# Optimization experiments

Hardware: AMD Instinct MI355X
Metric: run time of the kernel (lower is better)

The kernel has to match this reference:

```python
import jax, jax.numpy as jnp
import numpy as np

HEADS = 16  # init kwarg 'heads'

def setup_inputs() -> dict:
    key = jax.random.key(0)
    k1, k2, k3 = jax.random.split(key, 3)
    B, S, D = 2, 2048, 1024
    x = jax.random.normal(k1, (B, S, D), dtype=jnp.float32)
    # nn.Linear(dim, 3*dim, bias=False): y = x @ W^T; store as [D, 3D] already transposed.
    w_qkv = jax.random.normal(k2, (D, 3 * D), dtype=jnp.float32) * 0.02
    w_out = jax.random.normal(k3, (D, D), dtype=jnp.float32) * 0.02
    return {"x": x, "w_qkv": w_qkv, "w_out": w_out}

def reference(x, w_qkv, w_out):
    B, S, D = x.shape
    H = HEADS
    hd = D // H
    scale = 1.0 / jnp.sqrt(jnp.asarray(hd, dtype=x.dtype))
    qkv = x @ w_qkv                      # [B, S, 3D]
    q, k, v = jnp.split(qkv, 3, axis=-1)
    def to_heads(t):
        return t.reshape(B, S, H, hd).transpose(0, 2, 1, 3)  # [B, H, S, hd]
    q, k, v = to_heads(q), to_heads(k), to_heads(v)
    scores = jnp.einsum('bhqd,bhkd->bhqk', q, k) * scale      # [B, H, S, S]
    # causal mask: query i attends to keys j <= i
    causal = jnp.tril(jnp.ones((S, S), dtype=bool))
    scores = jnp.where(causal, scores, -jnp.inf)
    p = jax.nn.softmax(scores, axis=-1)  # online-softmax in the original == exact softmax
    o = jnp.einsum('bhqk,bhkd->bhqd', p, v)                   # [B, H, S, hd]
    out = o.transpose(0, 2, 1, 3).reshape(B, S, D)
    return out @ w_out
```

## Files before the change

### kernel.cpp

```cpp
#include <hip/hip_runtime.h>


typedef unsigned short u16;
typedef unsigned int   u32;
typedef __attribute__((ext_vector_type(4))) u16    u16x4;
typedef __attribute__((ext_vector_type(8))) u16    u16x8;
typedef __attribute__((ext_vector_type(4))) short  s16x4;
typedef __attribute__((ext_vector_type(8))) __bf16 bf16x8;
typedef __attribute__((ext_vector_type(4))) float  f32x4;
typedef __attribute__((ext_vector_type(16))) float f32x16;

#define DEV static __device__ __forceinline__

DEV u16 f2b(float f) {
  unsigned u = __float_as_uint(f);
  u += 0x7fffu + ((u >> 16) & 1u);
  return (u16)(u >> 16);
}

DEV void gload_lds16(const void* g, void* l) {
  __builtin_amdgcn_global_load_lds((const __attribute__((address_space(1))) void*)g,
                                   (__attribute__((address_space(3))) void*)l, 16, 0, 0);
}

DEV unsigned lds_off(const void* p) {
  return (unsigned)(unsigned long long)(const __attribute__((address_space(3))) void*)p;
}

DEV s16x4 tr_read(unsigned off) {
  s16x4 d;
  asm volatile("ds_read_b64_tr_b16 %0, %1" : "=v"(d) : "v"(off));
  return d;
}

DEV u32 cvt_pk(float lo, float hi) {
  u32 r;
  asm("v_cvt_pk_bf16_f32 %0, %1, %2" : "=v"(r) : "v"(lo), "v"(hi));
  return r;
}

DEV void pswap(u32& x, u32& y) {
  asm volatile("v_permlane32_swap_b32 %0, %1" : "+v"(x), "+v"(y));
}

DEV f32x4 mfma32(bf16x8 a, bf16x8 b, f32x4 c) {
  return __builtin_amdgcn_mfma_f32_16x16x32_bf16(a, b, c, 0, 0, 0);
}
DEV f32x16 mfma3232(bf16x8 a, bf16x8 b, f32x16 c) {
  return __builtin_amdgcn_mfma_f32_32x32x16_bf16(a, b, c, 0, 0, 0);
}

__global__ __launch_bounds__(256) void cvt_kernel(const float* __restrict__ in,
                                                  u16* __restrict__ out, int n4) {
  int i = blockIdx.x * 256 + threadIdx.x;
  if (i >= n4) return;
  const float4 v = ((const float4*)in)[i];
  u16x4 o = { f2b(v.x), f2b(v.y), f2b(v.z), f2b(v.w) };
  ((u16x4*)out)[i] = o;
}

__global__ __launch_bounds__(256) void transpose_cvt(const float* __restrict__ w,
                                                     u16* __restrict__ wt,
                                                     const int Kdim, const int Ndim,
                                                     const int scaleN) {
  __shared__ u16 ls[32][33];
  const int tn = blockIdx.x * 32, tk = blockIdx.y * 32;
  const int t = threadIdx.x;
  const int r = t >> 3, c4 = (t & 7) * 4;
  const float s = (tn < scaleN) ? 0.18033688011112042f : 1.0f;
  float4 v = *(const float4*)(w + (size_t)(tk + r) * Ndim + tn + c4);
  ls[r][c4 + 0] = f2b(v.x * s); ls[r][c4 + 1] = f2b(v.y * s);
  ls[r][c4 + 2] = f2b(v.z * s); ls[r][c4 + 3] = f2b(v.w * s);
  __syncthreads();
  u16x4 ov = { ls[c4 + 0][r], ls[c4 + 1][r], ls[c4 + 2][r], ls[c4 + 3][r] };
  *(u16x4*)(wt + (size_t)(tn + r) * Kdim + tk + c4) = ov;
}

template<bool OUT_BF16>
__global__ __launch_bounds__(256) void gemm_bt(const u16* __restrict__ A,
                                               const u16* __restrict__ Bt,
                                               void* __restrict__ C, const int ldc) {
  const int gx = gridDim.x;
  const int id = (int)(blockIdx.y * gx + blockIdx.x);
  const int nxp = gx >> 3;
  const int xcd = id & 7, loc = id >> 3;
  const int tn = (xcd * nxp + loc % nxp) * 128;
  const int tm = (loc / nxp) * 128;
  const int tid = threadIdx.x;
  const int wave = tid >> 6, lane = tid & 63;
  const int wr = wave >> 1, wc = wave & 1;
  const int lg = lane >> 4, lc = lane & 15;
  __shared__ __align__(128) u16 lsA[128 * 32];
  __shared__ __align__(128) u16 lsB[128 * 32];

  f32x4 acc[4][4];
#pragma unroll
  for (int i = 0; i < 4; ++i)
#pragma unroll
    for (int j = 0; j < 4; ++j) acc[i][j] = (f32x4){0.f, 0.f, 0.f, 0.f};

  for (int kt = 0; kt < 32; ++kt) {
#pragma unroll
    for (int c = 0; c < 2; ++c) {
      const int p = tid + c * 256;
      const int row = p >> 2, ck = p & 3;
      const int cg = ck ^ ((row >> 1) & 3);
      gload_lds16(A  + (size_t)(tm + row) * 1024 + kt * 32 + cg * 8, (char*)lsA + p * 16);
      gload_lds16(Bt + (size_t)(tn + row) * 1024 + kt * 32 + cg * 8, (char*)lsB + p * 16);
    }
    __syncthreads();
    bf16x8 af[4], bg[4];
#pragma unroll
    for (int i = 0; i < 4; ++i) {
      const int ar = wr * 64 + i * 16 + lc;
      af[i] = *(const bf16x8*)(lsA + ar * 32 + (lg ^ ((ar >> 1) & 3)) * 8);
      const int br = wc * 64 + i * 16 + lc;
      bg[i] = *(const bf16x8*)(lsB + br * 32 + (lg ^ ((br >> 1) & 3)) * 8);
    }
#pragma unroll
    for (int i = 0; i < 4; ++i)
#pragma unroll
      for (int j = 0; j < 4; ++j)
        acc[i][j] = mfma32(af[i], bg[j], acc[i][j]);
    __syncthreads();
  }

#pragma unroll
  for (int i = 0; i < 4; ++i) {
#pragma unroll
    for (int r = 0; r < 4; ++r) {
      const int m = tm + wr * 64 + i * 16 + lg * 4 + r;
#pragma unroll
      for (int j = 0; j < 4; ++j) {
        const int n = tn + wc * 64 + j * 16 + lc;
        if (OUT_BF16) ((u16*)C)[(size_t)m * ldc + n] = f2b(acc[i][j][r]);
        else          ((float*)C)[(size_t)m * ldc + n] = acc[i][j][r];
      }
    }
  }
}

__global__ __launch_bounds__(128, 2) void attn_kernel(const u16* __restrict__ qkv,
                                                      u16* __restrict__ o) {
  const int qb  = 63 - (int)(blockIdx.x >> 5);
  const int bh  = blockIdx.x & 31;
  const int b   = bh >> 4, h = bh & 15;
  const int tid  = threadIdx.x;
  const int wave = tid >> 6, lane = tid & 63;
  const int l31 = lane & 31, lg2 = lane >> 5;

  __shared__ __align__(128) char smem[2][8192];
  __shared__ float lsm[2][32];
  char* wb = smem[wave];
  const unsigned vb = lds_off(wb + 4096);

  const size_t bS = (size_t)b * 2048;
  const int T  = qb + 1;
  const int q0 = qb * 32;

  const u16* qrow = qkv + (bS + q0 + l31) * 3072 + h * 64;
  bf16x8 qf[4];
#pragma unroll
  for (int m = 0; m < 4; ++m)
    qf[m] = *(const bf16x8*)(qrow + 16 * m + 8 * lg2);

  unsigned koff[4], voff[4];
#pragma unroll
  for (int c = 0; c < 4; ++c) {
    const int p = c * 64 + lane;
    {
      const int row = p >> 3;
      const int cg = (p & 7) ^ (row & 7);
      koff[c] = (unsigned)(row * 3072 + 1024 + h * 64 + cg * 8);
    }
    {
      const int s = p >> 3, cw = p & 7;
      voff[c] = (unsigned)((4 * (s >> 2) + (cw >> 1)) * 3072 + 2048 + h * 64
                           + (s & 3) * 16 + (cw & 1) * 8);
    }
  }

  auto STAGE = [&](int t) {
    const u16* base = qkv + (bS + (size_t)t * 32) * 3072;
#pragma unroll
    for (int c = 0; c < 4; ++c)
      gload_lds16(base + koff[c], wb + (c * 64 + lane) * 16);
#pragma unroll
    for (int c = 0; c < 4; ++c)
      gload_lds16(base + voff[c], wb + 4096 + (c * 64 + lane) * 16);
  };

  float lsum = 0.f;
  f32x16 accO[2];
#pragma unroll
  for (int r = 0; r < 16; ++r) { accO[0][r] = 0.f; accO[1][r] = 0.f; }

  if (wave < T) STAGE(wave);

  for (int t = wave; t < T; t += 2) {
    asm volatile("s_waitcnt vmcnt(0)" ::: "memory");
    __builtin_amdgcn_sched_barrier(0);

    const u16* kbp = (const u16*)wb + l31 * 64;
    bf16x8 kf[4];
#pragma unroll
    for (int m = 0; m < 4; ++m)
      kf[m] = *(const bf16x8*)(kbp + (((2 * m + lg2) ^ (l31 & 7)) * 8));
    s16x4 vr[2][2][2];
#pragma unroll
    for (int db = 0; db < 2; ++db)
#pragma unroll
      for (int hh = 0; hh < 2; ++hh) {
        const unsigned a0 = vb +
          (unsigned)(((4 * hh + 2 * lg2) * 4 + db * 2 + (l31 >> 4)) * 128 + (l31 & 15) * 8);
        vr[db][hh][0] = tr_read(a0);
        vr[db][hh][1] = tr_read(a0 + 512);
      }
    asm volatile("s_waitcnt lgkmcnt(0)" ::: "memory");
    __builtin_amdgcn_sched_barrier(0);

    if (t + 2 < T) STAGE(t + 2);
    __builtin_amdgcn_sched_barrier(0);

    f32x16 sc;
#pragma unroll
    for (int r = 0; r < 16; ++r) sc[r] = 0.f;
    __builtin_amdgcn_s_setprio(1);
#pragma unroll
    for (int m = 0; m < 4; ++m)
      sc = mfma3232(kf[m], qf[m], sc);
    __builtin_amdgcn_s_setprio(0);

    float pp[16];
    if (t == T - 1) {
#pragma unroll
      for (int r = 0; r < 16; ++r) {
        const int kvp = (r & 3) + 8 * (r >> 2) + 4 * lg2;
        pp[r] = (kvp <= l31) ? exp2f(sc[r]) : 0.f;
      }
    } else {
#pragma unroll
      for (int r = 0; r < 16; ++r) pp[r] = exp2f(sc[r]);
    }
#pragma unroll
    for (int r = 0; r < 16; ++r) lsum += pp[r];

    u32 a01 = cvt_pk(pp[0], pp[1]),   a23 = cvt_pk(pp[2], pp[3]);
    u32 b01 = cvt_pk(pp[4], pp[5]),   b23 = cvt_pk(pp[6], pp[7]);
    u32 c01 = cvt_pk(pp[8], pp[9]),   c23 = cvt_pk(pp[10], pp[11]);
    u32 d01 = cvt_pk(pp[12], pp[13]), d23 = cvt_pk(pp[14], pp[15]);
    pswap(a01, b01); pswap(a23, b23);
    pswap(c01, d01); pswap(c23, d23);
    union Frag { u32 w[4]; bf16x8 v; };
    Frag f0, f1;
    f0.w[0] = a01; f0.w[1] = a23; f0.w[2] = b01; f0.w[3] = b23;
    f1.w[0] = c01; f1.w[1] = c23; f1.w[2] = d01; f1.w[3] = d23;

    __builtin_amdgcn_s_setprio(1);
#pragma unroll
    for (int db = 0; db < 2; ++db) {
      union { s16x4 hh[2]; bf16x8 v; } u0, u1;
      u0.hh[0] = vr[db][0][0]; u0.hh[1] = vr[db][0][1];
      u1.hh[0] = vr[db][1][0]; u1.hh[1] = vr[db][1][1];
      accO[db] = mfma3232(f0.v, u0.v, accO[db]);
      accO[db] = mfma3232(f1.v, u1.v, accO[db]);
    }
    __builtin_amdgcn_s_setprio(0);
  }

  lsum += __shfl_xor(lsum, 32);
  float* mO = (float*)wb;
#pragma unroll
  for (int db = 0; db < 2; ++db)
#pragma unroll
    for (int r = 0; r < 16; ++r) {
      const int qp = (r & 3) + 8 * (r >> 2) + 4 * lg2;
      mO[qp * 64 + db * 32 + l31] = accO[db][r];
    }
  if (lane < 32) lsm[wave][l31] = lsum;
  __syncthreads();

  const float* O0 = (const float*)smem[0];
  const float* O1 = (const float*)smem[1];
  const int q  = wave * 16 + (lane >> 2);
  const int d0 = (lane & 3) * 16;
  const float inv = 1.f / (lsm[0][q] + lsm[1][q]);
  u16x8 ov[2];
#pragma unroll
  for (int j = 0; j < 4; ++j) {
    const f32x4 a = *(const f32x4*)(O0 + q * 64 + d0 + j * 4);
    const f32x4 c = *(const f32x4*)(O1 + q * 64 + d0 + j * 4);
#pragma unroll
    for (int e = 0; e < 4; ++e)
      ov[j >> 1][(j & 1) * 4 + e] = f2b((a[e] + c[e]) * inv);
  }
  const size_t orow = (bS + q0 + q) * 1024 + h * 64 + d0;
  *(u16x8*)(o + orow)     = ov[0];
  *(u16x8*)(o + orow + 8) = ov[1];
}

extern "C" void kernel_launch(void* const* d_in, const int* in_sizes, int n_in,
                              void* d_out, int out_size, void* d_ws, size_t ws_size,
                              hipStream_t stream) {
  const float* x     = (const float*)d_in[0];
  const float* w_qkv = (const float*)d_in[1];
  const float* w_out = (const float*)d_in[2];
  float* out = (float*)d_out;
  char* ws = (char*)d_ws;

  u16* xb    = (u16*)(ws + 0);
  u16* wqkvT = (u16*)(ws + 8388608);
  u16* woutT = (u16*)(ws + 14680064);
  u16* qkvb  = (u16*)(ws + 16777216);
  u16* ob    = (u16*)(ws + 41943040);

  cvt_kernel<<<4096, 256, 0, stream>>>(x, xb, 1048576);
  transpose_cvt<<<dim3(96, 32), 256, 0, stream>>>(w_qkv, wqkvT, 1024, 3072, 1024);
  transpose_cvt<<<dim3(32, 32), 256, 0, stream>>>(w_out, woutT, 1024, 1024, 0);
  gemm_bt<true ><<<dim3(24, 32), 256, 0, stream>>>(xb, wqkvT, (void*)qkvb, 3072);
  attn_kernel<<<2048, 128, 0, stream>>>(qkvb, ob);
  gemm_bt<false><<<dim3(8, 32), 256, 0, stream>>>(ob, woutT, (void*)out, 1024);
}
```

Measured before the change: 111.0 us.

## Add 256x256-tile pipelined GEMM for the QKV projection

Replaces the generic gemm_bt launch for the QKV projection with a dedicated 512-thread kernel that computes 256x256 output tiles. It uses double-buffered LDS filled by direct global-to-LDS loads and an XOR-swizzled layout to avoid bank conflicts. Compute is split into four quadrant phases that interleave LDS fragment reads, next-tile prefetch, barriers and MFMA bursts raised with setprio. The larger tiles cut global traffic per FLOP and overlap loads with math, at the cost of 128KB of LDS per block, more barriers, high register pressure, and only 192 blocks to cover the GPU.

Result: slower. 113.5 us (+2.3%).

```diff
diff --git a/kernel.cpp b/kernel.cpp
--- a/kernel.cpp
+++ b/kernel.cpp
@@ -49,6 +49,12 @@
 DEV f32x16 mfma3232(bf16x8 a, bf16x8 b, f32x16 c) {
   return __builtin_amdgcn_mfma_f32_32x32x16_bf16(a, b, c, 0, 0, 0);
 }
+
+#define BAR()      __builtin_amdgcn_s_barrier()
+#define WAIT_LGKM0() do { asm volatile("s_waitcnt lgkmcnt(0)" ::: "memory"); \
+                          __builtin_amdgcn_sched_barrier(0); } while (0)
+#define WAIT_VM0()   do { asm volatile("s_waitcnt vmcnt(0)" ::: "memory");   \
+                          __builtin_amdgcn_sched_barrier(0); } while (0)
 
 __global__ __launch_bounds__(256) void cvt_kernel(const float* __restrict__ in,
                                                   u16* __restrict__ out, int n4) {
@@ -140,6 +146,166 @@
   }
 }
 
+__global__ __launch_bounds__(512, 2) void gemm256(const u16* __restrict__ A,
+                                                  const u16* __restrict__ Bt,
+                                                  u16* __restrict__ C, const int ldc) {
+  const int id  = (int)blockIdx.x;
+  const int lin = (id & 7) * 24 + (id >> 3);
+  const int tn  = (lin >> 4) * 256;
+  const int tm  = (lin & 15) * 256;
+  const int tid = (int)threadIdx.x;
+  const int lane = tid & 63, wid = tid >> 6;
+  const int wm = wid >> 2, wn = wid & 3;
+  const int lg = lane >> 4, lc = lane & 15;
+
+  __shared__ __align__(128) u16 lsA[2][256 * 64];
+  __shared__ __align__(128) u16 lsB[2][256 * 64];
+
+  f32x4 acc[8][4];
+#pragma unroll
+  for (int i = 0; i < 8; ++i)
+#pragma unroll
+    for (int j = 0; j < 4; ++j) acc[i][j] = (f32x4){0.f, 0.f, 0.f, 0.f};
+
+  unsigned asrc[4], bsrc[4], ldst[4];
+#pragma unroll
+  for (int c = 0; c < 4; ++c) {
+    const int ca = c * 512 + tid;
+    const int row = ca >> 3;
+    const int cg = (ca & 7) ^ (row & 7);
+    asrc[c] = (unsigned)((tm + row) * 1024 + cg * 8);
+    bsrc[c] = (unsigned)((tn + row) * 1024 + cg * 8);
+    ldst[c] = (unsigned)(ca * 16);
+  }
+
+  bf16x8 af[4][2], bg[2][2];
+
+#pragma unroll
+  for (int c = 0; c < 4; ++c) gload_lds16(A + asrc[c], (char*)lsA[0] + ldst[c]);
+#pragma unroll
+  for (int c = 0; c < 4; ++c) gload_lds16(Bt + bsrc[c], (char*)lsB[0] + ldst[c]);
+  WAIT_VM0();
+  BAR();
+
+  for (int t = 0; t < 16; ++t) {
+    const u16* bA = lsA[t & 1];
+    const u16* bB = lsB[t & 1];
+    char* sA = (char*)lsA[(t & 1) ^ 1];
+    char* sB = (char*)lsB[(t & 1) ^ 1];
+    const bool stg = (t < 15);
+    const unsigned koff = (unsigned)((t + 1) * 64);
+
+#pragma unroll
+    for (int i = 0; i < 4; ++i)
+#pragma unroll
+      for (int ks = 0; ks < 2; ++ks) {
+        const int row = wm * 128 + i * 16 + lc;
+        af[i][ks] = *(const bf16x8*)(bA + row * 64 + ((ks * 4 + lg) ^ (row & 7)) * 8);
+      }
+#pragma unroll
+    for (int j = 0; j < 2; ++j)
+#pragma unroll
+      for (int ks = 0; ks < 2; ++ks) {
+        const int row = wn * 64 + j * 16 + lc;
+        bg[j][ks] = *(const bf16x8*)(bB + row * 64 + ((ks * 4 + lg) ^ (row & 7)) * 8);
+      }
+    if (stg) {
+#pragma unroll
+      for (int c = 0; c < 4; ++c) gload_lds16(A + asrc[c] + koff, sA + ldst[c]);
+    }
+    BAR();
+    WAIT_LGKM0();
+    __builtin_amdgcn_s_setprio(1);
+#pragma unroll
+    for (int i = 0; i < 4; ++i)
+#pragma unroll
+      for (int j = 0; j < 2; ++j)
+#pragma unroll
+        for (int ks = 0; ks < 2; ++ks)
+          acc[i][j] = mfma32(af[i][ks], bg[j][ks], acc[i][j]);
+    __builtin_amdgcn_s_setprio(0);
+    BAR();
+
+#pragma unroll
+    for (int j = 0; j < 2; ++j)
+#pragma unroll
+      for (int ks = 0; ks < 2; ++ks) {
+        const int row = wn * 64 + 32 + j * 16 + lc;
+        bg[j][ks] = *(const bf16x8*)(bB + row * 64 + ((ks * 4 + lg) ^ (row & 7)) * 8);
+      }
+    if (stg) {
+#pragma unroll
+      for (int c = 0; c < 4; ++c) gload_lds16(Bt + bsrc[c] + koff, sB + ldst[c]);
+    }
+    BAR();
+    WAIT_LGKM0();
+    __builtin_amdgcn_s_setprio(1);
+#pragma unroll
+    for (int i = 0; i < 4; ++i)
+#pragma unroll
+      for (int j = 0; j < 2; ++j)
+#pragma unroll
+        for (int ks = 0; ks < 2; ++ks)
+          acc[i][2 + j] = mfma32(af[i][ks], bg[j][ks], acc[i][2 + j]);
+    __builtin_amdgcn_s_setprio(0);
+    BAR();
+
+#pragma unroll
+    for (int i = 0; i < 4; ++i)
+#pragma unroll
+      for (int ks = 0; ks < 2; ++ks) {
+        const int row = wm * 128 + 64 + i * 16 + lc;
+        af[i][ks] = *(const bf16x8*)(bA + row * 64 + ((ks * 4 + lg) ^ (row & 7)) * 8);
+      }
+    BAR();
+    WAIT_LGKM0();
+    __builtin_amdgcn_s_setprio(1);
+#pragma unroll
+    for (int i = 0; i < 4; ++i)
+#pragma unroll
+      for (int j = 0; j < 2; ++j)
+#pragma unroll
+        for (int ks = 0; ks < 2; ++ks)
+          acc[4 + i][2 + j] = mfma32(af[i][ks], bg[j][ks], acc[4 + i][2 + j]);
+    __builtin_amdgcn_s_setprio(0);
+    BAR();
+
+#pragma unroll
+    for (int j = 0; j < 2; ++j)
+#pragma unroll
+      for (int ks = 0; ks < 2; ++ks) {
+        const int row = wn * 64 + j * 16 + lc;
+        bg[j][ks] = *(const bf16x8*)(bB + row * 64 + ((ks * 4 + lg) ^ (row & 7)) * 8);
+      }
+    BAR();
+    WAIT_LGKM0();
+    __builtin_amdgcn_s_setprio(1);
+#pragma unroll
+    for (int i = 0; i < 4; ++i)
+#pragma unroll
+      for (int j = 0; j < 2; ++j)
+#pragma unroll
+        for (int ks = 0; ks < 2; ++ks)
+          acc[4 + i][j] = mfma32(af[i][ks], bg[j][ks], acc[4 + i][j]);
+    __builtin_amdgcn_s_setprio(0);
+    WAIT_VM0();
+    BAR();
+  }
+
+#pragma unroll
+  for (int mi = 0; mi < 8; ++mi) {
+#pragma unroll
+    for (int r = 0; r < 4; ++r) {
+      const int m = tm + wm * 128 + mi * 16 + lg * 4 + r;
+#pragma unroll
+      for (int nj = 0; nj < 4; ++nj) {
+        const int n = tn + wn * 64 + nj * 16 + lc;
+        C[(size_t)m * ldc + n] = f2b(acc[mi][nj][r]);
+      }
+    }
+  }
+}
+
 __global__ __launch_bounds__(128, 2) void attn_kernel(const u16* __restrict__ qkv,
                                                       u16* __restrict__ o) {
   const int qb  = 63 - (int)(blockIdx.x >> 5);
@@ -317,7 +483,7 @@
   cvt_kernel<<<4096, 256, 0, stream>>>(x, xb, 1048576);
   transpose_cvt<<<dim3(96, 32), 256, 0, stream>>>(w_qkv, wqkvT, 1024, 3072, 1024);
   transpose_cvt<<<dim3(32, 32), 256, 0, stream>>>(w_out, woutT, 1024, 1024, 0);
-  gemm_bt<true ><<<dim3(24, 32), 256, 0, stream>>>(xb, wqkvT, (void*)qkvb, 3072);
+  gemm256<<<192, 512, 0, stream>>>(xb, wqkvT, qkvb, 3072);
   attn_kernel<<<2048, 128, 0, stream>>>(qkvb, ob);
   gemm_bt<false><<<dim3(8, 32), 256, 0, stream>>>(ob, woutT, (void*)out, 1024);
 }
```

## Load K tiles directly into registers and halve attention LDS footprint

Applied to the files above, without the earlier changes.

K fragments are now loaded straight from global memory into registers, one tile ahead, instead of being staged through LDS. Only V goes through LDS, which halves per-wave LDS to 4 KB, and the score MFMAs are issued before the wait on the V load. The final combine now accumulates both waves' partial outputs into one 8 KB buffer in turn, which costs an extra barrier. The aim is lower LDS use, more room for blocks per CU and more overlap of loads with compute, at the cost of more registers and unswizzled direct global loads of K.

New measurement: 127.5 us. 1.15x slower.

```diff
diff --git a/kernel.cpp b/kernel.cpp
--- a/kernel.cpp
+++ b/kernel.cpp
@@ -149,10 +149,10 @@
   const int wave = tid >> 6, lane = tid & 63;
   const int l31 = lane & 31, lg2 = lane >> 5;
 
-  __shared__ __align__(128) char smem[2][8192];
+  __shared__ __align__(128) char smem[2][4096];
   __shared__ float lsm[2][32];
   char* wb = smem[wave];
-  const unsigned vb = lds_off(wb + 4096);
+  const unsigned vb = lds_off(wb);
 
   const size_t bS = (size_t)b * 2048;
   const int T  = qb + 1;
@@ -164,30 +164,28 @@
   for (int m = 0; m < 4; ++m)
     qf[m] = *(const bf16x8*)(qrow + 16 * m + 8 * lg2);
 
-  unsigned koff[4], voff[4];
+  const u16* krow = qkv + (bS + l31) * 3072 + 1024 + h * 64 + 8 * lg2;
+
+  unsigned voff[4];
 #pragma unroll
   for (int c = 0; c < 4; ++c) {
     const int p = c * 64 + lane;
-    {
-      const int row = p >> 3;
-      const int cg = (p & 7) ^ (row & 7);
-      koff[c] = (unsigned)(row * 3072 + 1024 + h * 64 + cg * 8);
-    }
-    {
-      const int s = p >> 3, cw = p & 7;
-      voff[c] = (unsigned)((4 * (s >> 2) + (cw >> 1)) * 3072 + 2048 + h * 64
-                           + (s & 3) * 16 + (cw & 1) * 8);
-    }
-  }
-
-  auto STAGE = [&](int t) {
+    const int s = p >> 3, cw = p & 7;
+    voff[c] = (unsigned)((4 * (s >> 2) + (cw >> 1)) * 3072 + 2048 + h * 64
+                         + (s & 3) * 16 + (cw & 1) * 8);
+  }
+
+  auto KLOAD = [&](int t, bf16x8* kd) {
+    const u16* kb = krow + (size_t)t * 32 * 3072;
+#pragma unroll
+    for (int m = 0; m < 4; ++m)
+      kd[m] = *(const bf16x8*)(kb + 16 * m);
+  };
+  auto VSTAGE = [&](int t) {
     const u16* base = qkv + (bS + (size_t)t * 32) * 3072;
 #pragma unroll
     for (int c = 0; c < 4; ++c)
-      gload_lds16(base + koff[c], wb + (c * 64 + lane) * 16);
-#pragma unroll
-    for (int c = 0; c < 4; ++c)
-      gload_lds16(base + voff[c], wb + 4096 + (c * 64 + lane) * 16);
+      gload_lds16(base + voff[c], wb + (c * 64 + lane) * 16);
   };
 
   float lsum = 0.f;
@@ -195,17 +193,31 @@
 #pragma unroll
   for (int r = 0; r < 16; ++r) { accO[0][r] = 0.f; accO[1][r] = 0.f; }
 
-  if (wave < T) STAGE(wave);
+  bf16x8 kfn[4];
+  if (wave < T) { KLOAD(wave, kfn); VSTAGE(wave); }
 
   for (int t = wave; t < T; t += 2) {
-    asm volatile("s_waitcnt vmcnt(0)" ::: "memory");
+    asm volatile("s_waitcnt vmcnt(4)" ::: "memory");
     __builtin_amdgcn_sched_barrier(0);
-
-    const u16* kbp = (const u16*)wb + l31 * 64;
     bf16x8 kf[4];
 #pragma unroll
+    for (int m = 0; m < 4; ++m) kf[m] = kfn[m];
+    const bool pre = (t + 2 < T);
+    if (pre) KLOAD(t + 2, kfn);
+
+    f32x16 sc;
+#pragma unroll
+    for (int r = 0; r < 16; ++r) sc[r] = 0.f;
+    __builtin_amdgcn_s_setprio(1);
+#pragma unroll
     for (int m = 0; m < 4; ++m)
-      kf[m] = *(const bf16x8*)(kbp + (((2 * m + lg2) ^ (l31 & 7)) * 8));
+      sc = mfma3232(kf[m], qf[m], sc);
+    __builtin_amdgcn_s_setprio(0);
+
+    if (pre) { asm volatile("s_waitcnt vmcnt(4)" ::: "memory"); }
+    else     { asm volatile("s_waitcnt vmcnt(0)" ::: "memory"); }
+    __builtin_amdgcn_sched_barrier(0);
+
     s16x4 vr[2][2][2];
 #pragma unroll
     for (int db = 0; db < 2; ++db)
@@ -218,18 +230,8 @@
       }
     asm volatile("s_waitcnt lgkmcnt(0)" ::: "memory");
     __builtin_amdgcn_sched_barrier(0);
-
-    if (t + 2 < T) STAGE(t + 2);
+    if (pre) VSTAGE(t + 2);
     __builtin_amdgcn_sched_barrier(0);
-
-    f32x16 sc;
-#pragma unroll
-    for (int r = 0; r < 16; ++r) sc[r] = 0.f;
-    __builtin_amdgcn_s_setprio(1);
-#pragma unroll
-    for (int m = 0; m < 4; ++m)
-      sc = mfma3232(kf[m], qf[m], sc);
-    __builtin_amdgcn_s_setprio(0);
 
     float pp[16];
     if (t == T - 1) {
@@ -269,30 +271,40 @@
   }
 
   lsum += __shfl_xor(lsum, 32);
-  float* mO = (float*)wb;
-#pragma unroll
-  for (int db = 0; db < 2; ++db)
-#pragma unroll
-    for (int r = 0; r < 16; ++r) {
-      const int qp = (r & 3) + 8 * (r >> 2) + 4 * lg2;
-      mO[qp * 64 + db * 32 + l31] = accO[db][r];
-    }
+  float* mO = (float*)&smem[0][0];
   if (lane < 32) lsm[wave][l31] = lsum;
   __syncthreads();
-
-  const float* O0 = (const float*)smem[0];
-  const float* O1 = (const float*)smem[1];
+  if (wave == 0) {
+#pragma unroll
+    for (int db = 0; db < 2; ++db)
+#pragma unroll
+      for (int r = 0; r < 16; ++r) {
+        const int qp = (r & 3) + 8 * (r >> 2) + 4 * lg2;
+        mO[qp * 64 + db * 32 + l31] = accO[db][r];
+      }
+  }
+  __syncthreads();
+  if (wave == 1) {
+#pragma unroll
+    for (int db = 0; db < 2; ++db)
+#pragma unroll
+      for (int r = 0; r < 16; ++r) {
+        const int qp = (r & 3) + 8 * (r >> 2) + 4 * lg2;
+        mO[qp * 64 + db * 32 + l31] += accO[db][r];
+      }
+  }
+  __syncthreads();
+
   const int q  = wave * 16 + (lane >> 2);
   const int d0 = (lane & 3) * 16;
   const float inv = 1.f / (lsm[0][q] + lsm[1][q]);
   u16x8 ov[2];
 #pragma unroll
   for (int j = 0; j < 4; ++j) {
-    const f32x4 a = *(const f32x4*)(O0 + q * 64 + d0 + j * 4);
-    const f32x4 c = *(const f32x4*)(O1 + q * 64 + d0 + j * 4);
+    const f32x4 a = *(const f32x4*)(mO + q * 64 + d0 + j * 4);
 #pragma unroll
     for (int e = 0; e < 4; ++e)
-      ov[j >> 1][(j & 1) * 4 + e] = f2b((a[e] + c[e]) * inv);
+      ov[j >> 1][(j & 1) * 4 + e] = f2b(a[e] * inv);
   }
   const size_t orow = (bS + q0 + q) * 1024 + h * 64 + d0;
   *(u16x8*)(o + orow)     = ov[0];
```

## Pair light and heavy causal query blocks in one 256-thread attention workgroup

Applied to the files above, without the earlier changes.

Each attention workgroup now has four waves and handles two query blocks: a short causal block p and the long mirror block 63-p, with two waves per block splitting the key tiles. The goal is to balance work per workgroup and halve the grid, which evens out the causal triangle across CUs. The epilogue now combines partial outputs by an in-place LDS add guarded by extra barriers, so the waves of the light block sit idle until the heavy block finishes.

Result: slower. 114.9 us (+3.5%).

```diff
diff --git a/kernel.cpp b/kernel.cpp
--- a/kernel.cpp
+++ b/kernel.cpp
@@ -140,21 +140,23 @@
   }
 }
 
-__global__ __launch_bounds__(128, 2) void attn_kernel(const u16* __restrict__ qkv,
+__global__ __launch_bounds__(256, 2) void attn_kernel(const u16* __restrict__ qkv,
                                                       u16* __restrict__ o) {
-  const int qb  = 63 - (int)(blockIdx.x >> 5);
+  const int p   = (int)(blockIdx.x >> 5);
   const int bh  = blockIdx.x & 31;
   const int b   = bh >> 4, h = bh & 15;
   const int tid  = threadIdx.x;
   const int wave = tid >> 6, lane = tid & 63;
+  const int wg = wave >> 1, wp = wave & 1;
   const int l31 = lane & 31, lg2 = lane >> 5;
 
-  __shared__ __align__(128) char smem[2][8192];
-  __shared__ float lsm[2][32];
+  __shared__ __align__(128) char smem[4][8192];
+  __shared__ float lsm[4][32];
   char* wb = smem[wave];
   const unsigned vb = lds_off(wb + 4096);
 
   const size_t bS = (size_t)b * 2048;
+  const int qb = wg ? (63 - p) : p;
   const int T  = qb + 1;
   const int q0 = qb * 32;
 
@@ -167,14 +169,14 @@
   unsigned koff[4], voff[4];
 #pragma unroll
   for (int c = 0; c < 4; ++c) {
-    const int p = c * 64 + lane;
+    const int pp_ = c * 64 + lane;
     {
-      const int row = p >> 3;
-      const int cg = (p & 7) ^ (row & 7);
+      const int row = pp_ >> 3;
+      const int cg = (pp_ & 7) ^ (row & 7);
       koff[c] = (unsigned)(row * 3072 + 1024 + h * 64 + cg * 8);
     }
     {
-      const int s = p >> 3, cw = p & 7;
+      const int s = pp_ >> 3, cw = pp_ & 7;
       voff[c] = (unsigned)((4 * (s >> 2) + (cw >> 1)) * 3072 + 2048 + h * 64
                            + (s & 3) * 16 + (cw & 1) * 8);
     }
@@ -195,9 +197,9 @@
 #pragma unroll
   for (int r = 0; r < 16; ++r) { accO[0][r] = 0.f; accO[1][r] = 0.f; }
 
-  if (wave < T) STAGE(wave);
-
-  for (int t = wave; t < T; t += 2) {
+  if (wp < T) STAGE(wp);
+
+  for (int t = wp; t < T; t += 2) {
     asm volatile("s_waitcnt vmcnt(0)" ::: "memory");
     __builtin_amdgcn_sched_barrier(0);
 
@@ -269,30 +271,40 @@
   }
 
   lsum += __shfl_xor(lsum, 32);
-  float* mO = (float*)wb;
-#pragma unroll
-  for (int db = 0; db < 2; ++db)
-#pragma unroll
-    for (int r = 0; r < 16; ++r) {
-      const int qp = (r & 3) + 8 * (r >> 2) + 4 * lg2;
-      mO[qp * 64 + db * 32 + l31] = accO[db][r];
-    }
   if (lane < 32) lsm[wave][l31] = lsum;
+  float* mO = (float*)smem[wg * 2];
   __syncthreads();
-
-  const float* O0 = (const float*)smem[0];
-  const float* O1 = (const float*)smem[1];
-  const int q  = wave * 16 + (lane >> 2);
+  if (wp == 0) {
+#pragma unroll
+    for (int db = 0; db < 2; ++db)
+#pragma unroll
+      for (int r = 0; r < 16; ++r) {
+        const int qp = (r & 3) + 8 * (r >> 2) + 4 * lg2;
+        mO[qp * 64 + db * 32 + l31] = accO[db][r];
+      }
+  }
+  __syncthreads();
+  if (wp == 1) {
+#pragma unroll
+    for (int db = 0; db < 2; ++db)
+#pragma unroll
+      for (int r = 0; r < 16; ++r) {
+        const int qp = (r & 3) + 8 * (r >> 2) + 4 * lg2;
+        mO[qp * 64 + db * 32 + l31] += accO[db][r];
+      }
+  }
+  __syncthreads();
+
+  const int q  = wp * 16 + (lane >> 2);
   const int d0 = (lane & 3) * 16;
-  const float inv = 1.f / (lsm[0][q] + lsm[1][q]);
+  const float inv = 1.f / (lsm[wg * 2][q] + lsm[wg * 2 + 1][q]);
   u16x8 ov[2];
 #pragma unroll
   for (int j = 0; j < 4; ++j) {
-    const f32x4 a = *(const f32x4*)(O0 + q * 64 + d0 + j * 4);
-    const f32x4 c = *(const f32x4*)(O1 + q * 64 + d0 + j * 4);
+    const f32x4 a = *(const f32x4*)(mO + q * 64 + d0 + j * 4);
 #pragma unroll
     for (int e = 0; e < 4; ++e)
-      ov[j >> 1][(j & 1) * 4 + e] = f2b((a[e] + c[e]) * inv);
+      ov[j >> 1][(j & 1) * 4 + e] = f2b(a[e] * inv);
   }
   const size_t orow = (bS + q0 + q) * 1024 + h * 64 + d0;
   *(u16x8*)(o + orow)     = ov[0];
@@ -318,6 +330,6 @@
   transpose_cvt<<<dim3(96, 32), 256, 0, stream>>>(w_qkv, wqkvT, 1024, 3072, 1024);
   transpose_cvt<<<dim3(32, 32), 256, 0, stream>>>(w_out, woutT, 1024, 1024, 0);
   gemm_bt<true ><<<dim3(24, 32), 256, 0, stream>>>(xb, wqkvT, (void*)qkvb, 3072);
-  attn_kernel<<<2048, 128, 0, stream>>>(qkvb, ob);
+  attn_kernel<<<1024, 256, 0, stream>>>(qkvb, ob);
   gemm_bt<false><<<dim3(8, 32), 256, 0, stream>>>(ob, woutT, (void*)out, 1024);
 }
```
